# Kernel optimization log

Measured on AMD Instinct MI355X. Metric: run time of the kernel, lower is better.

## Reference

```python
import jax, jax.numpy as jnp
import numpy as np

N_NODES, N_FEAT, HIDDEN, N_EDGES, N_GRAPHS = 50000, 128, 64, 800000, 64
BN_EPS = 1e-5


def setup_inputs() -> dict:
    key = jax.random.key(0)
    ks = jax.random.split(key, 12)
    x = jax.random.normal(ks[0], (N_NODES, N_FEAT), jnp.float32)
    edge_index = jax.random.randint(ks[1], (2, N_EDGES), 0, N_NODES, jnp.int32)
    batch = jnp.sort(jax.random.randint(ks[2], (N_NODES,), 0, N_GRAPHS, jnp.int32))
    s_in = 1.0 / np.sqrt(N_FEAT)
    s_h = 1.0 / np.sqrt(HIDDEN)
    return {
        "x": x,
        "edge_index": edge_index,
        "batch": batch,
        "W_in": jax.random.normal(ks[3], (HIDDEN, N_FEAT), jnp.float32) * s_in,
        "W1": jax.random.normal(ks[4], (HIDDEN, N_FEAT), jnp.float32) * s_in,
        "b1": jnp.zeros((HIDDEN,), jnp.float32),
        "Ws": jax.random.normal(ks[5], (4, HIDDEN, HIDDEN), jnp.float32) * s_h,
        "bs": jnp.zeros((4, HIDDEN), jnp.float32),
        "bn_gamma": jnp.ones((5, HIDDEN), jnp.float32),
        "bn_beta": jnp.zeros((5, HIDDEN), jnp.float32),
        "bn_mean": jnp.zeros((5, HIDDEN), jnp.float32),
        "bn_var": jnp.ones((5, HIDDEN), jnp.float32),
        "lin_w": jax.random.normal(ks[6], (1, HIDDEN), jnp.float32) * s_h,
        "lin_b": jnp.zeros((1,), jnp.float32),
    }


def reference(x, edge_index, batch, W_in, W1, b1, Ws, bs, bn_gamma, bn_beta, bn_mean, bn_var, lin_w, lin_b):
    N = x.shape[0]
    # add self loops (GCNConv default), symmetric normalization D^-1/2 (A+I) D^-1/2
    loop = jnp.arange(N, dtype=edge_index.dtype)
    src = jnp.concatenate([edge_index[0], loop])  # [E+N]
    dst = jnp.concatenate([edge_index[1], loop])
    deg = jax.ops.segment_sum(jnp.ones_like(dst, jnp.float32), dst, num_segments=N)
    dinv = jax.lax.rsqrt(deg)  # deg >= 1 due to self-loops
    norm = dinv[src] * dinv[dst]  # [E+N]

    def gcn(h, W, b):
        h = h @ W.T                          # [N, H]
        msg = h[src] * norm[:, None]          # gather + edge scaling
        out = jax.ops.segment_sum(msg, dst, num_segments=N)  # scatter-add
        return out + b

    def bn(h, i):
        # eval-mode BatchNorm1d with running stats
        return (h - bn_mean[i]) * (bn_gamma[i] * jax.lax.rsqrt(bn_var[i] + BN_EPS)) + bn_beta[i]

    identity = x @ W_in.T  # input projection for residual
    # layer 1 (dropout = identity in eval)
    h = jax.nn.relu(bn(gcn(x, W1, b1), 0)) + identity
    # layers 2-4 with residual
    for i in range(3):
        h = jax.nn.relu(bn(gcn(h, Ws[i], bs[i]), i + 1)) + h
    # layer 5, no residual afterwards
    h = jax.nn.relu(bn(gcn(h, Ws[3], bs[3]), 4))

    # global mean pool over graphs
    sums = jax.ops.segment_sum(h, batch, num_segments=N_GRAPHS)
    cnts = jax.ops.segment_sum(jnp.ones((N,), jnp.float32), batch, num_segments=N_GRAPHS)
    pooled = sums / jnp.maximum(cnts, 1.0)[:, None]  # [G, H]
    return pooled @ lin_w.T + lin_b  # [G, 1]
```

## Files before the change

### kernel.cpp

```cpp
#include <hip/hip_runtime.h>
#include <hip/hip_fp16.h>

#define N_NODES 50000
#define N_FEAT  128
#define HID     64
#define N_EDGES 800000
#define N_GRAPHS 64
#define MAXDEG  64
#define BN_EPS  1e-5f
#define NB256(n) (((n) + 255) / 256)

__global__ __launch_bounds__(256) void k_zero(int* fill) {
    int i = blockIdx.x * 256 + threadIdx.x;
    if (i < N_NODES) fill[i] = 0;
}

template <int K, bool HOUT>
__device__ __forceinline__ void gemm_body(int vb,
                                          const float* __restrict__ in,
                                          const float* __restrict__ W,
                                          float* __restrict__ outf,
                                          __half* __restrict__ outh,
                                          float4* Wt, float4* xs) {
    constexpr int K4 = K / 4;
    const int t = threadIdx.x;
    const int base = vb * 40;

    const float4* xv = (const float4*)(in + (long long)base * K);
    for (int i = t; i < 40 * K4; i += 256) xs[i] = xv[i];

    const float4* Wv = (const float4*)W;
    const int hh = t & 63;
    const int ng = t >> 6;
    float4 acc[10];
#pragma unroll
    for (int j = 0; j < 10; ++j) acc[j] = make_float4(0.f, 0.f, 0.f, 0.f);

    for (int c = 0; c < K4; c += 16) {
        __syncthreads();
        for (int i = t; i < HID * 16; i += 256) {
            int h2 = i >> 4, k4 = i & 15;
            Wt[k4 * 65 + h2] = Wv[h2 * K4 + c + k4];
        }
        __syncthreads();
#pragma unroll
        for (int k4 = 0; k4 < 16; ++k4) {
            float4 w = Wt[k4 * 65 + hh];
#pragma unroll
            for (int j = 0; j < 10; ++j) {
                float4 x = xs[(ng + 4 * j) * K4 + c + k4];
                acc[j].x += w.x * x.x;
                acc[j].y += w.y * x.y;
                acc[j].z += w.z * x.z;
                acc[j].w += w.w * x.w;
            }
        }
    }
#pragma unroll
    for (int j = 0; j < 10; ++j) {
        int node = base + ng + 4 * j;
        float v = acc[j].x + acc[j].y + acc[j].z + acc[j].w;
        if (HOUT) outh[node * HID + hh] = __float2half(v);
        else      outf[node * HID + hh] = v;
    }
}

#define GE_NB 2500
__global__ __launch_bounds__(256) void k_gemmedge(const int* __restrict__ ei,
                                                  int* fill, unsigned short* __restrict__ colp,
                                                  const float* __restrict__ x,
                                                  const float* __restrict__ W_in,
                                                  const float* __restrict__ W1,
                                                  float* __restrict__ h,
                                                  __half* __restrict__ g16) {
    __shared__ float4 Wt[16 * 65];
    __shared__ float4 xs[40 * 32];
    const int bid = blockIdx.x;
    const int t = threadIdx.x;

    const int ebase = bid * 320;
    int s1 = ei[ebase + t];
    int d1 = ei[N_EDGES + ebase + t];
    int k1 = atomicAdd(&fill[d1], 1);
    int s2 = 0, d2 = 0, k2 = MAXDEG;
    if (t < 64) {
        s2 = ei[ebase + 256 + t];
        d2 = ei[N_EDGES + ebase + 256 + t];
        k2 = atomicAdd(&fill[d2], 1);
    }

    if (bid < 1250)
        gemm_body<N_FEAT, false>(bid, x, W_in, h, nullptr, Wt, xs);
    else
        gemm_body<N_FEAT, true>(bid - 1250, x, W1, nullptr, g16, Wt, xs);

    if (k1 < MAXDEG) colp[d1 * MAXDEG + k1] = (unsigned short)s1;
    if (k2 < MAXDEG) colp[d2 * MAXDEG + k2] = (unsigned short)s2;
}

__device__ __forceinline__ void acc8s(const uint4 r, float* a, float s) {
    float2 f0 = __half22float2(*(const __half2*)&r.x);
    float2 f1 = __half22float2(*(const __half2*)&r.y);
    float2 f2 = __half22float2(*(const __half2*)&r.z);
    float2 f3 = __half22float2(*(const __half2*)&r.w);
    a[0] += s * f0.x; a[1] += s * f0.y; a[2] += s * f1.x; a[3] += s * f1.y;
    a[4] += s * f2.x; a[5] += s * f2.y; a[6] += s * f3.x; a[7] += s * f3.y;
}

template <bool NSCALE, bool DOGEMM>
__global__ __launch_bounds__(256) void k_gather_fused(const __half* __restrict__ gin,
                                                      const unsigned short* __restrict__ colp,
                                                      const int* __restrict__ fill,
                                                      const float* __restrict__ b,
                                                      const float* __restrict__ gamma,
                                                      const float* __restrict__ beta,
                                                      const float* __restrict__ mean,
                                                      const float* __restrict__ var,
                                                      const float4* __restrict__ res4,
                                                      float4* __restrict__ h4,
                                                      const float* __restrict__ W,
                                                      __half* __restrict__ gout) {
    __shared__ float4 Wt[DOGEMM ? 16 * 65 : 1];
    __shared__ float4 hrow[DOGEMM ? 4 * 16 : 1];

    const int t = threadIdx.x;
    const int wv = t >> 6;
    const int lane = t & 63;
    const int hh8 = lane & 7;
    const int sub = lane >> 3;
    const int n = blockIdx.x * 4 + wv;

    if (DOGEMM) {
        const float4* Wv = (const float4*)W;
        for (int i = t; i < HID * 16; i += 256) {
            int h2 = i >> 4, k4 = i & 15;
            Wt[k4 * 65 + h2] = Wv[i];
        }
        __syncthreads();
    }

    const uint4* gv = (const uint4*)gin;
    int fl = fill[n];
    int deg = fl < MAXDEG ? fl : MAXDEG;

    const bool valid = (lane < deg);
    int call = valid ? (int)colp[n * MAXDEG + lane] : n;
    float sall;
    if (NSCALE) sall = valid ? rsqrtf((float)fill[call] + 1.0f) : 0.0f;
    else        sall = valid ? 1.0f : 0.0f;

    float a[8];
#pragma unroll
    for (int i = 0; i < 8; ++i) a[i] = 0.f;

    int nr = (deg + 7) >> 3;
#pragma unroll 4
    for (int r = 0; r < nr; ++r) {
        int j = r * 8 + sub;
        int c = __shfl(call, j);
        float s = __shfl(sall, j);
        acc8s(gv[c * 8 + hh8], a, s);
    }

#pragma unroll
    for (int m = 8; m <= 32; m <<= 1) {
#pragma unroll
        for (int i = 0; i < 8; ++i) a[i] += __shfl_xor(a[i], m);
    }

    const float di = rsqrtf((float)fl + 1.0f);
    acc8s(gv[n * 8 + hh8], a, NSCALE ? di : 1.0f);

    float4 b0 = ((const float4*)b)[hh8 * 2],     b1 = ((const float4*)b)[hh8 * 2 + 1];
    float4 g0 = ((const float4*)gamma)[hh8 * 2], g1 = ((const float4*)gamma)[hh8 * 2 + 1];
    float4 e0 = ((const float4*)beta)[hh8 * 2],  e1 = ((const float4*)beta)[hh8 * 2 + 1];
    float4 m0 = ((const float4*)mean)[hh8 * 2],  m1 = ((const float4*)mean)[hh8 * 2 + 1];
    float4 v0 = ((const float4*)var)[hh8 * 2],   v1 = ((const float4*)var)[hh8 * 2 + 1];

    float bb[8] = {b0.x, b0.y, b0.z, b0.w, b1.x, b1.y, b1.z, b1.w};
    float gg[8] = {g0.x, g0.y, g0.z, g0.w, g1.x, g1.y, g1.z, g1.w};
    float ee[8] = {e0.x, e0.y, e0.z, e0.w, e1.x, e1.y, e1.z, e1.w};
    float mm[8] = {m0.x, m0.y, m0.z, m0.w, m1.x, m1.y, m1.z, m1.w};
    float vv[8] = {v0.x, v0.y, v0.z, v0.w, v1.x, v1.y, v1.z, v1.w};

    float o[8];
#pragma unroll
    for (int i = 0; i < 8; ++i) {
        float val = (a[i] * di + bb[i] - mm[i]) * (gg[i] * rsqrtf(vv[i] + BN_EPS)) + ee[i];
        o[i] = fmaxf(val, 0.f);
    }
    if (res4) {
        float4 r0 = res4[n * 16 + hh8 * 2];
        float4 r1 = res4[n * 16 + hh8 * 2 + 1];
        o[0] += r0.x; o[1] += r0.y; o[2] += r0.z; o[3] += r0.w;
        o[4] += r1.x; o[5] += r1.y; o[6] += r1.z; o[7] += r1.w;
    }
    float4 lo = make_float4(o[0], o[1], o[2], o[3]);
    float4 hi = make_float4(o[4], o[5], o[6], o[7]);
    if (sub == 0) {
        h4[n * 16 + hh8 * 2]     = lo;
        h4[n * 16 + hh8 * 2 + 1] = hi;
        if (DOGEMM) {
            hrow[wv * 16 + hh8 * 2]     = lo;
            hrow[wv * 16 + hh8 * 2 + 1] = hi;
        }
    }

    if (DOGEMM) {
        const int hh = lane;
        float4 acc = make_float4(0.f, 0.f, 0.f, 0.f);
#pragma unroll
        for (int k4 = 0; k4 < 16; ++k4) {
            float4 hv = hrow[wv * 16 + k4];
            float4 wvv = Wt[k4 * 65 + hh];
            acc.x += hv.x * wvv.x;
            acc.y += hv.y * wvv.y;
            acc.z += hv.z * wvv.z;
            acc.w += hv.w * wvv.w;
        }
        float v = (acc.x + acc.y + acc.z + acc.w) * di;
        gout[n * HID + hh] = __float2half(v);
    }
}

__device__ __forceinline__ int lowerb(const int* __restrict__ b, int val) {
    int lo = 0, hi = N_NODES;
    while (lo < hi) {
        int mid = (lo + hi) >> 1;
        if (b[mid] < val) lo = mid + 1; else hi = mid;
    }
    return lo;
}

__global__ __launch_bounds__(1024) void k_poolfinal(const float* __restrict__ h,
                                                    const int* __restrict__ batch,
                                                    const float* __restrict__ lin_w,
                                                    const float* __restrict__ lin_b,
                                                    float* __restrict__ out) {
    __shared__ float red[16][HID];
    int g = blockIdx.x;
    int w = threadIdx.x >> 6;
    int hh = threadIdx.x & 63;
    int start = lowerb(batch, g);
    int end = lowerb(batch, g + 1);
    int len = end - start;
    float acc = 0.f;
    for (int n = start + w; n < end; n += 16) acc += h[n * HID + hh];
    red[w][hh] = acc;
    __syncthreads();
    if (w == 0) {
        float s = 0.f;
#pragma unroll
        for (int i = 0; i < 16; ++i) s += red[i][hh];
        float c = fmaxf((float)len, 1.0f);
        float v = (s / c) * lin_w[hh];
#pragma unroll
        for (int off = 32; off > 0; off >>= 1) v += __shfl_down(v, off);
        if (hh == 0) out[g] = v + lin_b[0];
    }
}

extern "C" void kernel_launch(void* const* d_in, const int* in_sizes, int n_in,
                              void* d_out, int out_size, void* d_ws, size_t ws_size,
                              hipStream_t stream) {
    const float* x     = (const float*)d_in[0];
    const int*   ei    = (const int*)d_in[1];
    const int*   batch = (const int*)d_in[2];
    const float* W_in  = (const float*)d_in[3];
    const float* W1    = (const float*)d_in[4];
    const float* b1    = (const float*)d_in[5];
    const float* Ws    = (const float*)d_in[6];
    const float* bs_   = (const float*)d_in[7];
    const float* bn_g  = (const float*)d_in[8];
    const float* bn_b  = (const float*)d_in[9];
    const float* bn_m  = (const float*)d_in[10];
    const float* bn_v  = (const float*)d_in[11];
    const float* lin_w = (const float*)d_in[12];
    const float* lin_b = (const float*)d_in[13];
    float* out = (float*)d_out;

    char* q = (char*)d_ws;
    int*            fill = (int*)q;             q += (size_t)50048 * 4;
    unsigned short* colp = (unsigned short*)q;  q += (size_t)N_NODES * MAXDEG * 2;
    __half*         g16a = (__half*)q;          q += (size_t)N_NODES * HID * 2;
    __half*         g16b = (__half*)q;          q += (size_t)N_NODES * HID * 2;
    float*          h    = (float*)q;           q += (size_t)N_NODES * HID * 4;

    const int NB_N  = NB256(N_NODES);
    const int NB_GA = (N_NODES + 3) / 4;
    float4* h4 = (float4*)h;

    k_zero<<<NB_N, 256, 0, stream>>>(fill);
    k_gemmedge<<<GE_NB, 256, 0, stream>>>(ei, fill, colp, x, W_in, W1, h, g16a);

    k_gather_fused<true, true><<<NB_GA, 256, 0, stream>>>(
        g16a, colp, fill, b1, bn_g, bn_b, bn_m, bn_v,
        (const float4*)h, h4, Ws + 0 * HID * HID, g16b);

    k_gather_fused<false, true><<<NB_GA, 256, 0, stream>>>(
        g16b, colp, fill, bs_ + 0 * HID,
        bn_g + 1 * HID, bn_b + 1 * HID, bn_m + 1 * HID, bn_v + 1 * HID,
        (const float4*)h, h4, Ws + 1 * HID * HID, g16a);

    k_gather_fused<false, true><<<NB_GA, 256, 0, stream>>>(
        g16a, colp, fill, bs_ + 1 * HID,
        bn_g + 2 * HID, bn_b + 2 * HID, bn_m + 2 * HID, bn_v + 2 * HID,
        (const float4*)h, h4, Ws + 2 * HID * HID, g16b);

    k_gather_fused<false, true><<<NB_GA, 256, 0, stream>>>(
        g16b, colp, fill, bs_ + 2 * HID,
        bn_g + 3 * HID, bn_b + 3 * HID, bn_m + 3 * HID, bn_v + 3 * HID,
        (const float4*)h, h4, Ws + 3 * HID * HID, g16a);

    k_gather_fused<false, false><<<NB_GA, 256, 0, stream>>>(
        g16a, colp, fill, bs_ + 3 * HID,
        bn_g + 4 * HID, bn_b + 4 * HID, bn_m + 4 * HID, bn_v + 4 * HID,
        nullptr, h4, nullptr, nullptr);

    k_poolfinal<<<N_GRAPHS, 1024, 0, stream>>>(h, batch, lin_w, lin_b, out);
}
```

Baseline: 388.3 us.

## Process two destination nodes per wavefront in fused gather kernels

Each 64-lane wavefront now handles two nodes instead of one. Each half-wave loads up to 32 neighbor indices, and degrees above 32 fall back to a strided loop that reads the indices directly. Both nodes' gathers are interleaved, and the epilogue GEMM reuses each LDS weight load for both rows. This cuts the grid size in half and is meant to improve memory-level parallelism and weight reuse, at the cost of more registers and divergent tail loops. N_NODES/8 blocks exactly covers the nodes because 50000 is divisible by 8.

```diff
diff --git a/kernel.cpp b/kernel.cpp
--- a/kernel.cpp
+++ b/kernel.cpp
@@ -121,14 +121,15 @@
                                                       const float* __restrict__ W,
                                                       __half* __restrict__ gout) {
     __shared__ float4 Wt[DOGEMM ? 16 * 65 : 1];
-    __shared__ float4 hrow[DOGEMM ? 4 * 16 : 1];
+    __shared__ float4 hrow[DOGEMM ? 8 * 16 : 1];
 
     const int t = threadIdx.x;
     const int wv = t >> 6;
     const int lane = t & 63;
     const int hh8 = lane & 7;
     const int sub = lane >> 3;
-    const int n = blockIdx.x * 4 + wv;
+    const int nA = blockIdx.x * 8 + wv * 2;
+    const int nB = nA + 1;
 
     if (DOGEMM) {
         const float4* Wv = (const float4*)W;
@@ -140,36 +141,67 @@
     }
 
     const uint4* gv = (const uint4*)gin;
-    int fl = fill[n];
-    int deg = fl < MAXDEG ? fl : MAXDEG;
-
-    const bool valid = (lane < deg);
-    int call = valid ? (int)colp[n * MAXDEG + lane] : n;
+    int flA = fill[nA], flB = fill[nB];
+    int degA = flA < MAXDEG ? flA : MAXDEG;
+    int degB = flB < MAXDEG ? flB : MAXDEG;
+
+    const int myn   = (lane < 32) ? nA : nB;
+    const int myj   = lane & 31;
+    const int mydeg = (lane < 32) ? degA : degB;
+    const bool valid = (myj < mydeg);
+    int call = valid ? (int)colp[myn * MAXDEG + myj] : myn;
     float sall;
     if (NSCALE) sall = valid ? rsqrtf((float)fill[call] + 1.0f) : 0.0f;
     else        sall = valid ? 1.0f : 0.0f;
 
-    float a[8];
-#pragma unroll
-    for (int i = 0; i < 8; ++i) a[i] = 0.f;
-
-    int nr = (deg + 7) >> 3;
+    float aA[8], aB[8];
+#pragma unroll
+    for (int i = 0; i < 8; ++i) { aA[i] = 0.f; aB[i] = 0.f; }
+
+    int dA32 = degA < 32 ? degA : 32;
+    int dB32 = degB < 32 ? degB : 32;
+    int nra = (dA32 + 7) >> 3;
+    int nrb = (dB32 + 7) >> 3;
+    int nr = nra > nrb ? nra : nrb;
 #pragma unroll 4
     for (int r = 0; r < nr; ++r) {
         int j = r * 8 + sub;
-        int c = __shfl(call, j);
-        float s = __shfl(sall, j);
-        acc8s(gv[c * 8 + hh8], a, s);
+        if (r < nra) {
+            int c = __shfl(call, j);
+            float s = __shfl(sall, j);
+            acc8s(gv[c * 8 + hh8], aA, s);
+        }
+        if (r < nrb) {
+            int c = __shfl(call, 32 + j);
+            float s = __shfl(sall, 32 + j);
+            acc8s(gv[c * 8 + hh8], aB, s);
+        }
+    }
+    if (degA > 32) {
+        for (int j = 32 + sub; j < degA; j += 8) {
+            int c = (int)colp[nA * MAXDEG + j];
+            float s = NSCALE ? rsqrtf((float)fill[c] + 1.0f) : 1.0f;
+            acc8s(gv[c * 8 + hh8], aA, s);
+        }
+    }
+    if (degB > 32) {
+        for (int j = 32 + sub; j < degB; j += 8) {
+            int c = (int)colp[nB * MAXDEG + j];
+            float s = NSCALE ? rsqrtf((float)fill[c] + 1.0f) : 1.0f;
+            acc8s(gv[c * 8 + hh8], aB, s);
+        }
     }
 
 #pragma unroll
     for (int m = 8; m <= 32; m <<= 1) {
 #pragma unroll
-        for (int i = 0; i < 8; ++i) a[i] += __shfl_xor(a[i], m);
-    }
-
-    const float di = rsqrtf((float)fl + 1.0f);
-    acc8s(gv[n * 8 + hh8], a, NSCALE ? di : 1.0f);
+        for (int i = 0; i < 8; ++i) { aA[i] += __shfl_xor(aA[i], m); aB[i] += __shfl_xor(aB[i], m); }
+    }
+
+    const float diA = rsqrtf((float)flA + 1.0f);
+    const float diB = rsqrtf((float)flB + 1.0f);
+    acc8s(gv[nA * 8 + hh8], aA, NSCALE ? diA : 1.0f);
+    acc8s(gv[nB * 8 + hh8], aB, NSCALE ? diB : 1.0f);
 
     float4 b0 = ((const float4*)b)[hh8 * 2],     b1 = ((const float4*)b)[hh8 * 2 + 1];
     float4 g0 = ((const float4*)gamma)[hh8 * 2], g1 = ((const float4*)gamma)[hh8 * 2 + 1];
@@ -183,43 +215,56 @@
     float mm[8] = {m0.x, m0.y, m0.z, m0.w, m1.x, m1.y, m1.z, m1.w};
     float vv[8] = {v0.x, v0.y, v0.z, v0.w, v1.x, v1.y, v1.z, v1.w};
 
-    float o[8];
+    float oA[8], oB[8];
 #pragma unroll
     for (int i = 0; i < 8; ++i) {
-        float val = (a[i] * di + bb[i] - mm[i]) * (gg[i] * rsqrtf(vv[i] + BN_EPS)) + ee[i];
-        o[i] = fmaxf(val, 0.f);
+        float sc = gg[i] * rsqrtf(vv[i] + BN_EPS);
+        float vA = (aA[i] * diA + bb[i] - mm[i]) * sc + ee[i];
+        float vB = (aB[i] * diB + bb[i] - mm[i]) * sc + ee[i];
+        oA[i] = fmaxf(vA, 0.f);
+        oB[i] = fmaxf(vB, 0.f);
     }
     if (res4) {
-        float4 r0 = res4[n * 16 + hh8 * 2];
-        float4 r1 = res4[n * 16 + hh8 * 2 + 1];
-        o[0] += r0.x; o[1] += r0.y; o[2] += r0.z; o[3] += r0.w;
-        o[4] += r1.x; o[5] += r1.y; o[6] += r1.z; o[7] += r1.w;
-    }
-    float4 lo = make_float4(o[0], o[1], o[2], o[3]);
-    float4 hi = make_float4(o[4], o[5], o[6], o[7]);
+        float4 rA0 = res4[nA * 16 + hh8 * 2], rA1 = res4[nA * 16 + hh8 * 2 + 1];
+        float4 rB0 = res4[nB * 16 + hh8 * 2], rB1 = res4[nB * 16 + hh8 * 2 + 1];
+        oA[0] += rA0.x; oA[1] += rA0.y; oA[2] += rA0.z; oA[3] += rA0.w;
+        oA[4] += rA1.x; oA[5] += rA1.y; oA[6] += rA1.z; oA[7] += rA1.w;
+        oB[0] += rB0.x; oB[1] += rB0.y; oB[2] += rB0.z; oB[3] += rB0.w;
+        oB[4] += rB1.x; oB[5] += rB1.y; oB[6] += rB1.z; oB[7] += rB1.w;
+    }
+    float4 loA = make_float4(oA[0], oA[1], oA[2], oA[3]);
+    float4 hiA = make_float4(oA[4], oA[5], oA[6], oA[7]);
+    float4 loB = make_float4(oB[0], oB[1], oB[2], oB[3]);
+    float4 hiB = make_float4(oB[4], oB[5], oB[6], oB[7]);
     if (sub == 0) {
-        h4[n * 16 + hh8 * 2]     = lo;
-        h4[n * 16 + hh8 * 2 + 1] = hi;
+        h4[nA * 16 + hh8 * 2]     = loA;
+        h4[nA * 16 + hh8 * 2 + 1] = hiA;
+        h4[nB * 16 + hh8 * 2]     = loB;
+        h4[nB * 16 + hh8 * 2 + 1] = hiB;
         if (DOGEMM) {
-            hrow[wv * 16 + hh8 * 2]     = lo;
-            hrow[wv * 16 + hh8 * 2 + 1] = hi;
+            hrow[(wv * 2) * 16 + hh8 * 2]         = loA;
+            hrow[(wv * 2) * 16 + hh8 * 2 + 1]     = hiA;
+            hrow[(wv * 2 + 1) * 16 + hh8 * 2]     = loB;
+            hrow[(wv * 2 + 1) * 16 + hh8 * 2 + 1] = hiB;
         }
     }
 
     if (DOGEMM) {
         const int hh = lane;
-        float4 acc = make_float4(0.f, 0.f, 0.f, 0.f);
+        float4 accA = make_float4(0.f, 0.f, 0.f, 0.f);
+        float4 accB = make_float4(0.f, 0.f, 0.f, 0.f);
 #pragma unroll
         for (int k4 = 0; k4 < 16; ++k4) {
-            float4 hv = hrow[wv * 16 + k4];
-            float4 wvv = Wt[k4 * 65 + hh];
-            acc.x += hv.x * wvv.x;
-            acc.y += hv.y * wvv.y;
-            acc.z += hv.z * wvv.z;
-            acc.w += hv.w * wvv.w;
-        }
-        float v = (acc.x + acc.y + acc.z + acc.w) * di;
-        gout[n * HID + hh] = __float2half(v);
+            float4 w = Wt[k4 * 65 + hh];
+            float4 hA = hrow[(wv * 2) * 16 + k4];
+            float4 hB = hrow[(wv * 2 + 1) * 16 + k4];
+            accA.x += hA.x * w.x; accA.y += hA.y * w.y;
+            accA.z += hA.z * w.z; accA.w += hA.w * w.w;
+            accB.x += hB.x * w.x; accB.y += hB.y * w.y;
+            accB.z += hB.z * w.z; accB.w += hB.w * w.w;
+        }
+        gout[nA * HID + hh] = __float2half((accA.x + accA.y + accA.z + accA.w) * diA);
+        gout[nB * HID + hh] = __float2half((accB.x + accB.y + accB.z + accB.w) * diB);
     }
 }
 
@@ -286,33 +331,33 @@
     __half*         g16b = (__half*)q;          q += (size_t)N_NODES * HID * 2;
     float*          h    = (float*)q;           q += (size_t)N_NODES * HID * 4;
 
-    const int NB_N  = NB256(N_NODES);
-    const int NB_GA = (N_NODES + 3) / 4;
+    const int NB_N   = NB256(N_NODES);
+    const int NB_GA2 = N_NODES / 8;
     float4* h4 = (float4*)h;
 
     k_zero<<<NB_N, 256, 0, stream>>>(fill);
     k_gemmedge<<<GE_NB, 256, 0, stream>>>(ei, fill, colp, x, W_in, W1, h, g16a);
 
-    k_gather_fused<true, true><<<NB_GA, 256, 0, stream>>>(
+    k_gather_fused<true, true><<<NB_GA2, 256, 0, stream>>>(
         g16a, colp, fill, b1, bn_g, bn_b, bn_m, bn_v,
         (const float4*)h, h4, Ws + 0 * HID * HID, g16b);
 
-    k_gather_fused<false, true><<<NB_GA, 256, 0, stream>>>(
+    k_gather_fused<false, true><<<NB_GA2, 256, 0, stream>>>(
         g16b, colp, fill, bs_ + 0 * HID,
         bn_g + 1 * HID, bn_b + 1 * HID, bn_m + 1 * HID, bn_v + 1 * HID,
         (const float4*)h, h4, Ws + 1 * HID * HID, g16a);
 
-    k_gather_fused<false, true><<<NB_GA, 256, 0, stream>>>(
+    k_gather_fused<false, true><<<NB_GA2, 256, 0, stream>>>(
         g16a, colp, fill, bs_ + 1 * HID,
         bn_g + 2 * HID, bn_b + 2 * HID, bn_m + 2 * HID, bn_v + 2 * HID,
         (const float4*)h, h4, Ws + 2 * HID * HID, g16b);
 
-    k_gather_fused<false, true><<<NB_GA, 256, 0, stream>>>(
+    k_gather_fused<false, true><<<NB_GA2, 256, 0, stream>>>(
         g16b, colp, fill, bs_ + 2 * HID,
         bn_g + 3 * HID, bn_b + 3 * HID, bn_m + 3 * HID, bn_v + 3 * HID,
         (const float4*)h, h4, Ws + 3 * HID * HID, g16a);
 
-    k_gather_fused<false, false><<<NB_GA, 256, 0, stream>>>(
+    k_gather_fused<false, false><<<NB_GA2, 256, 0, stream>>>(
         g16a, colp, fill, bs_ + 3 * HID,
         bn_g + 4 * HID, bn_b + 4 * HID, bn_m + 4 * HID, bn_v + 4 * HID,
         nullptr, h4, nullptr, nullptr);
```

Measured after the change: 364.1 us. -6.2%, faster.

## Process four nodes per wavefront in fused GCN gather kernel

Applied to the files above, without the earlier changes.

Each wavefront now handles four destination nodes instead of one. Two half-wave neighbor lists are loaded per node pair, degrees above 32 go through a slow path, and gather loads for all four nodes are interleaved to raise memory-level parallelism. The W tile staged in shared memory is reused across 16 nodes per block instead of 4, which amortises its load. The BN scale and shift are precomputed once per lane. In exchange, register pressure rises from holding four 8-wide accumulators, the shuffle reduction does four times the work per wave, and the grid shrinks to N/16 blocks.

```diff
diff --git a/kernel.cpp b/kernel.cpp
--- a/kernel.cpp
+++ b/kernel.cpp
@@ -121,14 +121,14 @@
                                                       const float* __restrict__ W,
                                                       __half* __restrict__ gout) {
     __shared__ float4 Wt[DOGEMM ? 16 * 65 : 1];
-    __shared__ float4 hrow[DOGEMM ? 4 * 16 : 1];
+    __shared__ float4 hrow[DOGEMM ? 16 * 16 : 1];
 
     const int t = threadIdx.x;
     const int wv = t >> 6;
     const int lane = t & 63;
     const int hh8 = lane & 7;
     const int sub = lane >> 3;
-    const int n = blockIdx.x * 4 + wv;
+    const int nbase = blockIdx.x * 16 + wv * 4;
 
     if (DOGEMM) {
         const float4* Wv = (const float4*)W;
@@ -140,86 +140,142 @@
     }
 
     const uint4* gv = (const uint4*)gin;
-    int fl = fill[n];
-    int deg = fl < MAXDEG ? fl : MAXDEG;
-
-    const bool valid = (lane < deg);
-    int call = valid ? (int)colp[n * MAXDEG + lane] : n;
-    float sall;
-    if (NSCALE) sall = valid ? rsqrtf((float)fill[call] + 1.0f) : 0.0f;
-    else        sall = valid ? 1.0f : 0.0f;
-
-    float a[8];
-#pragma unroll
-    for (int i = 0; i < 8; ++i) a[i] = 0.f;
-
-    int nr = (deg + 7) >> 3;
-#pragma unroll 4
-    for (int r = 0; r < nr; ++r) {
+    int fls[4], degs[4];
+#pragma unroll
+    for (int i = 0; i < 4; ++i) {
+        fls[i] = fill[nbase + i];
+        degs[i] = fls[i] < MAXDEG ? fls[i] : MAXDEG;
+    }
+
+    const int half = lane >> 5;
+    const int myj = lane & 31;
+    const int n01 = nbase + half,     n23 = nbase + 2 + half;
+    const int dg01 = degs[half],      dg23 = degs[2 + half];
+    const bool v01 = (myj < dg01),    v23 = (myj < dg23);
+    int call01 = v01 ? (int)colp[n01 * MAXDEG + myj] : n01;
+    int call23 = v23 ? (int)colp[n23 * MAXDEG + myj] : n23;
+    float sall01, sall23;
+    if (NSCALE) {
+        sall01 = v01 ? rsqrtf((float)fill[call01] + 1.0f) : 0.0f;
+        sall23 = v23 ? rsqrtf((float)fill[call23] + 1.0f) : 0.0f;
+    } else {
+        sall01 = v01 ? 1.0f : 0.0f;
+        sall23 = v23 ? 1.0f : 0.0f;
+    }
+
+    float a[4][8];
+#pragma unroll
+    for (int i = 0; i < 4; ++i)
+#pragma unroll
+        for (int k = 0; k < 8; ++k) a[i][k] = 0.f;
+
+    int nrr[4];
+#pragma unroll
+    for (int i = 0; i < 4; ++i) {
+        int d32 = degs[i] < 32 ? degs[i] : 32;
+        nrr[i] = (d32 + 7) >> 3;
+    }
+    int nrmax = nrr[0];
+#pragma unroll
+    for (int i = 1; i < 4; ++i) nrmax = nrr[i] > nrmax ? nrr[i] : nrmax;
+
+#pragma unroll 2
+    for (int r = 0; r < nrmax; ++r) {
         int j = r * 8 + sub;
-        int c = __shfl(call, j);
-        float s = __shfl(sall, j);
-        acc8s(gv[c * 8 + hh8], a, s);
+        if (r < nrr[0]) { int c = __shfl(call01, j);      float s = __shfl(sall01, j);      acc8s(gv[c * 8 + hh8], a[0], s); }
+        if (r < nrr[1]) { int c = __shfl(call01, 32 + j); float s = __shfl(sall01, 32 + j); acc8s(gv[c * 8 + hh8], a[1], s); }
+        if (r < nrr[2]) { int c = __shfl(call23, j);      float s = __shfl(sall23, j);      acc8s(gv[c * 8 + hh8], a[2], s); }
+        if (r < nrr[3]) { int c = __shfl(call23, 32 + j); float s = __shfl(sall23, 32 + j); acc8s(gv[c * 8 + hh8], a[3], s); }
+    }
+#pragma unroll
+    for (int i = 0; i < 4; ++i) {
+        if (degs[i] > 32) {
+            int n = nbase + i;
+            for (int j = 32 + sub; j < degs[i]; j += 8) {
+                int c = (int)colp[n * MAXDEG + j];
+                float s = NSCALE ? rsqrtf((float)fill[c] + 1.0f) : 1.0f;
+                acc8s(gv[c * 8 + hh8], a[i], s);
+            }
+        }
     }
 
 #pragma unroll
     for (int m = 8; m <= 32; m <<= 1) {
 #pragma unroll
-        for (int i = 0; i < 8; ++i) a[i] += __shfl_xor(a[i], m);
-    }
-
-    const float di = rsqrtf((float)fl + 1.0f);
-    acc8s(gv[n * 8 + hh8], a, NSCALE ? di : 1.0f);
-
-    float4 b0 = ((const float4*)b)[hh8 * 2],     b1 = ((const float4*)b)[hh8 * 2 + 1];
-    float4 g0 = ((const float4*)gamma)[hh8 * 2], g1 = ((const float4*)gamma)[hh8 * 2 + 1];
-    float4 e0 = ((const float4*)beta)[hh8 * 2],  e1 = ((const float4*)beta)[hh8 * 2 + 1];
-    float4 m0 = ((const float4*)mean)[hh8 * 2],  m1 = ((const float4*)mean)[hh8 * 2 + 1];
-    float4 v0 = ((const float4*)var)[hh8 * 2],   v1 = ((const float4*)var)[hh8 * 2 + 1];
-
-    float bb[8] = {b0.x, b0.y, b0.z, b0.w, b1.x, b1.y, b1.z, b1.w};
-    float gg[8] = {g0.x, g0.y, g0.z, g0.w, g1.x, g1.y, g1.z, g1.w};
-    float ee[8] = {e0.x, e0.y, e0.z, e0.w, e1.x, e1.y, e1.z, e1.w};
-    float mm[8] = {m0.x, m0.y, m0.z, m0.w, m1.x, m1.y, m1.z, m1.w};
-    float vv[8] = {v0.x, v0.y, v0.z, v0.w, v1.x, v1.y, v1.z, v1.w};
-
-    float o[8];
-#pragma unroll
-    for (int i = 0; i < 8; ++i) {
-        float val = (a[i] * di + bb[i] - mm[i]) * (gg[i] * rsqrtf(vv[i] + BN_EPS)) + ee[i];
-        o[i] = fmaxf(val, 0.f);
-    }
-    if (res4) {
-        float4 r0 = res4[n * 16 + hh8 * 2];
-        float4 r1 = res4[n * 16 + hh8 * 2 + 1];
-        o[0] += r0.x; o[1] += r0.y; o[2] += r0.z; o[3] += r0.w;
-        o[4] += r1.x; o[5] += r1.y; o[6] += r1.z; o[7] += r1.w;
-    }
-    float4 lo = make_float4(o[0], o[1], o[2], o[3]);
-    float4 hi = make_float4(o[4], o[5], o[6], o[7]);
-    if (sub == 0) {
-        h4[n * 16 + hh8 * 2]     = lo;
-        h4[n * 16 + hh8 * 2 + 1] = hi;
-        if (DOGEMM) {
-            hrow[wv * 16 + hh8 * 2]     = lo;
-            hrow[wv * 16 + hh8 * 2 + 1] = hi;
+        for (int i = 0; i < 4; ++i)
+#pragma unroll
+            for (int k = 0; k < 8; ++k) a[i][k] += __shfl_xor(a[i][k], m);
+    }
+
+    float di[4];
+#pragma unroll
+    for (int i = 0; i < 4; ++i) di[i] = rsqrtf((float)fls[i] + 1.0f);
+#pragma unroll
+    for (int i = 0; i < 4; ++i)
+        acc8s(gv[(nbase + i) * 8 + hh8], a[i], NSCALE ? di[i] : 1.0f);
+
+    float sc[8], base8[8];
+    {
+        float4 b0 = ((const float4*)b)[hh8 * 2],     b1 = ((const float4*)b)[hh8 * 2 + 1];
+        float4 g0 = ((const float4*)gamma)[hh8 * 2], g1 = ((const float4*)gamma)[hh8 * 2 + 1];
+        float4 e0 = ((const float4*)beta)[hh8 * 2],  e1 = ((const float4*)beta)[hh8 * 2 + 1];
+        float4 m0 = ((const float4*)mean)[hh8 * 2],  m1 = ((const float4*)mean)[hh8 * 2 + 1];
+        float4 v0 = ((const float4*)var)[hh8 * 2],   v1 = ((const float4*)var)[hh8 * 2 + 1];
+        float bb[8] = {b0.x, b0.y, b0.z, b0.w, b1.x, b1.y, b1.z, b1.w};
+        float gg[8] = {g0.x, g0.y, g0.z, g0.w, g1.x, g1.y, g1.z, g1.w};
+        float ee[8] = {e0.x, e0.y, e0.z, e0.w, e1.x, e1.y, e1.z, e1.w};
+        float mm[8] = {m0.x, m0.y, m0.z, m0.w, m1.x, m1.y, m1.z, m1.w};
+        float vv[8] = {v0.x, v0.y, v0.z, v0.w, v1.x, v1.y, v1.z, v1.w};
+#pragma unroll
+        for (int k = 0; k < 8; ++k) {
+            sc[k] = gg[k] * rsqrtf(vv[k] + BN_EPS);
+            base8[k] = (bb[k] - mm[k]) * sc[k] + ee[k];
+        }
+    }
+
+#pragma unroll
+    for (int i = 0; i < 4; ++i) {
+        int n = nbase + i;
+        float dsc;
+        float o[8];
+#pragma unroll
+        for (int k = 0; k < 8; ++k) {
+            dsc = di[i] * sc[k];
+            o[k] = fmaxf(a[i][k] * dsc + base8[k], 0.f);
+        }
+        if (res4) {
+            float4 r0 = res4[n * 16 + hh8 * 2];
+            float4 r1 = res4[n * 16 + hh8 * 2 + 1];
+            o[0] += r0.x; o[1] += r0.y; o[2] += r0.z; o[3] += r0.w;
+            o[4] += r1.x; o[5] += r1.y; o[6] += r1.z; o[7] += r1.w;
+        }
+        float4 lo = make_float4(o[0], o[1], o[2], o[3]);
+        float4 hi = make_float4(o[4], o[5], o[6], o[7]);
+        if (sub == 0) {
+            h4[n * 16 + hh8 * 2]     = lo;
+            h4[n * 16 + hh8 * 2 + 1] = hi;
+            if (DOGEMM) {
+                hrow[(wv * 4 + i) * 16 + hh8 * 2]     = lo;
+                hrow[(wv * 4 + i) * 16 + hh8 * 2 + 1] = hi;
+            }
         }
     }
 
     if (DOGEMM) {
         const int hh = lane;
-        float4 acc = make_float4(0.f, 0.f, 0.f, 0.f);
-#pragma unroll
-        for (int k4 = 0; k4 < 16; ++k4) {
-            float4 hv = hrow[wv * 16 + k4];
-            float4 wvv = Wt[k4 * 65 + hh];
-            acc.x += hv.x * wvv.x;
-            acc.y += hv.y * wvv.y;
-            acc.z += hv.z * wvv.z;
-            acc.w += hv.w * wvv.w;
-        }
-        float v = (acc.x + acc.y + acc.z + acc.w) * di;
-        gout[n * HID + hh] = __float2half(v);
+#pragma unroll
+        for (int i = 0; i < 4; ++i) {
+            float4 acc = make_float4(0.f, 0.f, 0.f, 0.f);
+#pragma unroll
+            for (int k4 = 0; k4 < 16; ++k4) {
+                float4 hv = hrow[(wv * 4 + i) * 16 + k4];
+                float4 w = Wt[k4 * 65 + hh];
+                acc.x += hv.x * w.x; acc.y += hv.y * w.y;
+                acc.z += hv.z * w.z; acc.w += hv.w * w.w;
+            }
+            gout[(nbase + i) * HID + hh] =
+                __float2half((acc.x + acc.y + acc.z + acc.w) * di[i]);
+        }
     }
 }
 
@@ -286,33 +342,33 @@
     __half*         g16b = (__half*)q;          q += (size_t)N_NODES * HID * 2;
     float*          h    = (float*)q;           q += (size_t)N_NODES * HID * 4;
 
-    const int NB_N  = NB256(N_NODES);
-    const int NB_GA = (N_NODES + 3) / 4;
+    const int NB_N   = NB256(N_NODES);
+    const int NB_GA4 = N_NODES / 16;
     float4* h4 = (float4*)h;
 
     k_zero<<<NB_N, 256, 0, stream>>>(fill);
     k_gemmedge<<<GE_NB, 256, 0, stream>>>(ei, fill, colp, x, W_in, W1, h, g16a);
 
-    k_gather_fused<true, true><<<NB_GA, 256, 0, stream>>>(
+    k_gather_fused<true, true><<<NB_GA4, 256, 0, stream>>>(
         g16a, colp, fill, b1, bn_g, bn_b, bn_m, bn_v,
         (const float4*)h, h4, Ws + 0 * HID * HID, g16b);
 
-    k_gather_fused<false, true><<<NB_GA, 256, 0, stream>>>(
+    k_gather_fused<false, true><<<NB_GA4, 256, 0, stream>>>(
         g16b, colp, fill, bs_ + 0 * HID,
         bn_g + 1 * HID, bn_b + 1 * HID, bn_m + 1 * HID, bn_v + 1 * HID,
         (const float4*)h, h4, Ws + 1 * HID * HID, g16a);
 
-    k_gather_fused<false, true><<<NB_GA, 256, 0, stream>>>(
+    k_gather_fused<false, true><<<NB_GA4, 256, 0, stream>>>(
         g16a, colp, fill, bs_ + 1 * HID,
         bn_g + 2 * HID, bn_b + 2 * HID, bn_m + 2 * HID, bn_v + 2 * HID,
         (const float4*)h, h4, Ws + 2 * HID * HID, g16b);
 
-    k_gather_fused<false, true><<<NB_GA, 256, 0, stream>>>(
+    k_gather_fused<false, true><<<NB_GA4, 256, 0, stream>>>(
         g16b, colp, fill, bs_ + 2 * HID,
         bn_g + 3 * HID, bn_b + 3 * HID, bn_m + 3 * HID, bn_v + 3 * HID,
         (const float4*)h, h4, Ws + 3 * HID * HID, g16a);
 
-    k_gather_fused<false, false><<<NB_GA, 256, 0, stream>>>(
+    k_gather_fused<false, false><<<NB_GA4, 256, 0, stream>>>(
         g16a, colp, fill, bs_ + 3 * HID,
         bn_g + 4 * HID, bn_b + 4 * HID, bn_m + 4 * HID, bn_v + 4 * HID,
         nullptr, h4, nullptr, nullptr);
```

Measured after the change: 536.5 us. 1.38x slower.
